# Performance work log

Hardware: AMD Instinct MI355X
Metric: run time of the kernel (lower is better)

Reference implementation:

```python
import jax, jax.numpy as jnp
import numpy as np

N = 65536      # total nodes in batched graph
E = 524288     # total edges (avg degree 8)
DIN = 128
DOUT = 128
G = 512        # number of graphs in the batch
NC = 10        # n_class


def _glorot(k, fi, fo):
    lim = np.sqrt(6.0 / (fi + fo)).astype(np.float32)
    return jax.random.uniform(k, (fi, fo), jnp.float32, -lim, lim)


def setup_inputs() -> dict:
    key = jax.random.key(0)
    ks = jax.random.split(key, 16)
    inp = {
        "hx": jax.random.normal(ks[0], (N, DIN), jnp.float32),
        "src": jax.random.randint(ks[1], (E,), 0, N),
        "dst": jax.random.randint(ks[2], (E,), 0, N),
        "graph_id": jnp.sort(jax.random.randint(ks[3], (N,), 0, G)),
        "num_graphs": G,
    }
    dims = [(DIN, DOUT)] + [(DOUT, DOUT)] * 5
    for i, (fi, fo) in enumerate(dims):
        inp[f"W{i+1}"] = _glorot(ks[4 + i], fi, fo)
        inp[f"b{i+1}"] = jnp.zeros((fo,), jnp.float32)
    inp["Wp1"] = _glorot(ks[10], DOUT, DOUT // 2)
    inp["bp1"] = jnp.zeros((DOUT // 2,), jnp.float32)
    inp["Wp2"] = _glorot(ks[11], DOUT // 2, NC)
    inp["bp2"] = jnp.zeros((NC,), jnp.float32)
    return inp


def reference(hx, src, dst, graph_id, num_graphs,
              W1, b1, W2, b2, W3, b3, W4, b4, W5, b5, W6, b6,
              Wp1, bp1, Wp2, bp2):
    n = hx.shape[0]
    ones_e = jnp.ones((src.shape[0],), jnp.float32)
    # DGL GraphConv norm='both': D_out^{-1/2} on src side, D_in^{-1/2} on dst side,
    # degrees clamped to min 1 (allow_zero_in_degree=True).
    deg_out = jax.ops.segment_sum(ones_e, src, num_segments=n)
    deg_in = jax.ops.segment_sum(ones_e, dst, num_segments=n)
    norm_src = jax.lax.rsqrt(jnp.maximum(deg_out, 1.0))[:, None]
    norm_dst = jax.lax.rsqrt(jnp.maximum(deg_in, 1.0))[:, None]

    def gconv(x, W, b):
        m = (x * norm_src)[src]                                  # [E, d] gather
        agg = jax.ops.segment_sum(m, dst, num_segments=n)        # scatter-add
        return (agg * norm_dst) @ W + b

    # 6 stacked conv layers, ReLU; dropout is identity in eval mode
    h = hx
    for W, b in ((W1, b1), (W2, b2), (W3, b3), (W4, b4), (W5, b5), (W6, b6)):
        h = jax.nn.relu(gconv(h, W, b))

    # dgl.mean_nodes: per-graph mean pooling
    pooled = jax.ops.segment_sum(h, graph_id, num_segments=num_graphs)
    cnt = jax.ops.segment_sum(jnp.ones((n,), jnp.float32), graph_id,
                              num_segments=num_graphs)
    pooled = pooled / jnp.maximum(cnt, 1.0)[:, None]

    # pred_lin MLP head
    scores = jax.nn.relu(pooled @ Wp1 + bp1) @ Wp2 + bp2
    # Note: the trailing update_all writes graph.ndata['h'] only (side effect),
    # it does not affect the returned scores, so it is omitted.
    return scores
```

## Files before the change

### kernel.cpp

```cpp
#include <hip/hip_runtime.h>
#include <hip/hip_bf16.h>

#define NN 65536
#define NE 524288
#define DF 128
#define NG 512
#define NCLS 10
#define NBLK 256
#define EPB (NE / NBLK)
#define EPT (EPB / 256)

typedef __bf16 bf16x8 __attribute__((ext_vector_type(8)));
typedef float f32x4 __attribute__((ext_vector_type(4)));
typedef ushort u16x8 __attribute__((ext_vector_type(8)));

__device__ __forceinline__ float bl(uint x) { return __uint_as_float(x << 16); }
__device__ __forceinline__ float bh(uint x) { return __uint_as_float(x & 0xffff0000u); }
__device__ __forceinline__ ushort f2b(float f) {
    uint u = __float_as_uint(f);
    return (ushort)((u + 0x7fffu + ((u >> 16) & 1u)) >> 16);
}


__global__ __launch_bounds__(256) void k_hist(
        const int* __restrict__ src, const int* __restrict__ dst,
        int* __restrict__ Md, int* __restrict__ Ms) {
    __shared__ int hd[256], hs[256];
    int t = threadIdx.x, b = blockIdx.x;
    hd[t] = 0; hs[t] = 0;
    __syncthreads();
    int base = b * EPB;
    for (int k = 0; k < EPT; k++) {
        int e = base + k * 256 + t;
        atomicAdd(&hd[dst[e] >> 8], 1);
        atomicAdd(&hs[src[e] >> 8], 1);
    }
    __syncthreads();
    Md[b * 256 + t] = hd[t];
    Ms[b * 256 + t] = hs[t];
}

__global__ __launch_bounds__(256) void k_colscan(
        const int* __restrict__ Md, const int* __restrict__ Ms,
        int* __restrict__ Bd, int* __restrict__ Bs,
        int* __restrict__ bbd, int* __restrict__ bbs) {
    __shared__ int tot[256];
    int t = threadIdx.x;
    const int* M = blockIdx.x ? Ms : Md;
    int* B = blockIdx.x ? Bs : Bd;
    int* bb = blockIdx.x ? bbs : bbd;
    int run = 0;
    #pragma unroll 16
    for (int b = 0; b < NBLK; b++) { B[b * 256 + t] = run; run += M[b * 256 + t]; }
    tot[t] = run;
    __syncthreads();
    if (t == 0) { int r = 0; for (int i = 0; i < 256; i++) { int c = tot[i]; tot[i] = r; r += c; } }
    __syncthreads();
    bb[t] = tot[t];
    if (t == 0) bb[256] = NE;
}

__global__ __launch_bounds__(256) void k_place(
        const int* __restrict__ src, const int* __restrict__ dst,
        const int* __restrict__ Bd, const int* __restrict__ bbd,
        const int* __restrict__ Bs, const int* __restrict__ bbs,
        uint* __restrict__ drec, ushort* __restrict__ srec) {
    __shared__ int cd[256], cs[256];
    int t = threadIdx.x, b = blockIdx.x;
    cd[t] = bbd[t] + Bd[b * 256 + t];
    cs[t] = bbs[t] + Bs[b * 256 + t];
    __syncthreads();
    int base = b * EPB;
    for (int k = 0; k < EPT; k++) {
        int e = base + k * 256 + t;
        int d = dst[e], s = src[e];
        int pd = atomicAdd(&cd[d >> 8], 1);
        drec[pd] = ((uint)s << 8) | (uint)(d & 255);
        int ps = atomicAdd(&cs[s >> 8], 1);
        srec[ps] = (ushort)(s & 255);
    }
}

__global__ __launch_bounds__(256) void k_bshist(
        const uint* __restrict__ drec, const int* __restrict__ bbd,
        const ushort* __restrict__ srec, const int* __restrict__ bbs,
        int* __restrict__ col, int* __restrict__ rp,
        float* __restrict__ nd, float* __restrict__ ns) {
    __shared__ int hist[256], cur[256], sc[256];
    __shared__ uint recs[4096];
    __shared__ int colst[4096];
    int t = threadIdx.x;
    if (blockIdx.x >= 256) {
        int b = blockIdx.x - 256;
        hist[t] = 0;
        __syncthreads();
        int s0 = bbs[b], e0 = bbs[b + 1];
        for (int i = s0 + t; i < e0; i += 256)
            atomicAdd(&hist[srec[i] & 255], 1);
        __syncthreads();
        ns[b * 256 + t] = rsqrtf((float)max(hist[t], 1));
        return;
    }
    int b = blockIdx.x;
    int s0 = bbd[b];
    int n = min(bbd[b + 1] - s0, 4096);
    hist[t] = 0;
    __syncthreads();
    for (int i = t; i < n; i += 256) {
        uint rc = drec[s0 + i];
        recs[i] = rc;
        atomicAdd(&hist[rc & 255u], 1);
    }
    __syncthreads();
    int v = hist[t];
    sc[t] = v;
    __syncthreads();
    for (int off = 1; off < 256; off <<= 1) {
        int x = (t >= off) ? sc[t - off] : 0;
        __syncthreads();
        sc[t] += x;
        __syncthreads();
    }
    int excl = sc[t] - v;
    rp[b * 256 + t] = s0 + excl;
    nd[b * 256 + t] = rsqrtf((float)max(v, 1));
    cur[t] = excl;
    __syncthreads();
    for (int i = t; i < n; i += 256) {
        uint rc = recs[i];
        int p = atomicAdd(&cur[rc & 255u], 1);
        colst[p] = (int)(rc >> 8);
    }
    __syncthreads();
    for (int i = t; i < n; i += 256) col[s0 + i] = colst[i];
    if (b == 0) {
        if (t == 0) rp[NN] = NE;
        if (t < 64) col[NE + t] = 0;
    }
}

__global__ __launch_bounds__(256) void k_scale_wconv(
        const float* __restrict__ hx, const float* __restrict__ ns,
        uint2* __restrict__ xs2,
        const float* __restrict__ W0, const float* __restrict__ W1,
        const float* __restrict__ W2, const float* __restrict__ W3,
        const float* __restrict__ W4, const float* __restrict__ W5,
        ushort* __restrict__ Wt) {
    if (blockIdx.x < 8192) {
        int i = blockIdx.x * 256 + threadIdx.x;
        float4 v = ((const float4*)hx)[i];
        float s = ns[i >> 5];
        uint2 o;
        o.x = (uint)f2b(v.x * s) | ((uint)f2b(v.y * s) << 16);
        o.y = (uint)f2b(v.z * s) | ((uint)f2b(v.w * s) << 16);
        xs2[i] = o;
    } else {
        int t = (blockIdx.x - 8192) * 256 + threadIdx.x;
        int l = t >> 14, r = t & 16383;
        const float* W = l == 0 ? W0 : l == 1 ? W1 : l == 2 ? W2
                       : l == 3 ? W3 : l == 4 ? W4 : W5;
        int n = r >> 7, k = r & 127;
        Wt[l * 16384 + n * 128 + k] = f2b(W[k * 128 + n]);
    }
}

#define ISSUE4(x0, x1, x2, x3, CR, K) { \
    int c0_ = __builtin_amdgcn_readlane((int)(CR), (K)); \
    int c1_ = __builtin_amdgcn_readlane((int)(CR), (K) + 1); \
    int c2_ = __builtin_amdgcn_readlane((int)(CR), (K) + 2); \
    int c3_ = __builtin_amdgcn_readlane((int)(CR), (K) + 3); \
    x0 = X32[(size_t)c0_ * 64 + lane]; \
    x1 = X32[(size_t)c1_ * 64 + lane]; \
    x2 = X32[(size_t)c2_ * 64 + lane]; \
    x3 = X32[(size_t)c3_ * 64 + lane]; }

#define FLUSHROWS(J) \
    while ((J) >= next_e && r < 15) { \
        *(float2*)&Af[r * 132 + 2 * lane] = make_float2(a0, a1); \
        a0 = 0.f; a1 = 0.f; r++; \
        next_e = __builtin_amdgcn_readlane(rpv, r + 1); }

#define PROC1(xv, J) { FLUSHROWS(J) \
    if ((J) < E) { a0 += bl(xv); a1 += bh(xv); } }

__global__ __launch_bounds__(64, 2) void k_fused(
        const uint* __restrict__ X32,
        const int* __restrict__ rp, const int* __restrict__ col,
        const float* __restrict__ nd, const float* __restrict__ ns,
        const uint4* __restrict__ Wg,
        const float* __restrict__ b, int do_scale,
        ushort* __restrict__ out) {
    __shared__ float Af[16 * 132];
    int lane = threadIdx.x;
    int rr = lane & 15;
    int q = lane >> 4;
    int nb = blockIdx.x * 16;

    int rpv = rp[nb + (lane < 16 ? lane : 16)];
    int S = __builtin_amdgcn_readlane(rpv, 0);
    int E = __builtin_amdgcn_readlane(rpv, 16);
    int r = 0;
    int next_e = __builtin_amdgcn_readlane(rpv, 1);
    float a0 = 0.f, a1 = 0.f;

    int c0 = col[S + rr];
    int cA = col[S + 16 + rr];

    uint xa0, xa1, xa2, xa3, xb0, xb1, xb2, xb3;
    uint xc0, xc1, xc2, xc3, xd0, xd1, xd2, xd3;
    int j = S;
    ISSUE4(xa0, xa1, xa2, xa3, c0, 0)
    ISSUE4(xb0, xb1, xb2, xb3, c0, 4)
    ISSUE4(xc0, xc1, xc2, xc3, c0, 8)
    ISSUE4(xd0, xd1, xd2, xd3, c0, 12)
    for (; j + 16 <= E; j += 16) {
        int cF = col[j + 32 + rr];
        PROC1(xa0, j)      PROC1(xa1, j + 1)  PROC1(xa2, j + 2)  PROC1(xa3, j + 3)
        ISSUE4(xa0, xa1, xa2, xa3, cA, 0)
        PROC1(xb0, j + 4)  PROC1(xb1, j + 5)  PROC1(xb2, j + 6)  PROC1(xb3, j + 7)
        ISSUE4(xb0, xb1, xb2, xb3, cA, 4)
        PROC1(xc0, j + 8)  PROC1(xc1, j + 9)  PROC1(xc2, j + 10) PROC1(xc3, j + 11)
        ISSUE4(xc0, xc1, xc2, xc3, cA, 8)
        PROC1(xd0, j + 12) PROC1(xd1, j + 13) PROC1(xd2, j + 14) PROC1(xd3, j + 15)
        ISSUE4(xd0, xd1, xd2, xd3, cA, 12)
        cA = cF;
    }
    PROC1(xa0, j)      PROC1(xa1, j + 1)  PROC1(xa2, j + 2)  PROC1(xa3, j + 3)
    PROC1(xb0, j + 4)  PROC1(xb1, j + 5)  PROC1(xb2, j + 6)  PROC1(xb3, j + 7)
    PROC1(xc0, j + 8)  PROC1(xc1, j + 9)  PROC1(xc2, j + 10) PROC1(xc3, j + 11)
    PROC1(xd0, j + 12) PROC1(xd1, j + 13) PROC1(xd2, j + 14) PROC1(xd3, j + 15)
    for (; r < 16; r++) {
        *(float2*)&Af[r * 132 + 2 * lane] = make_float2(a0, a1);
        a0 = 0.f; a1 = 0.f;
    }

    float ndv = nd[nb + rr];
    bf16x8 afr[4];
    #pragma unroll
    for (int ks = 0; ks < 4; ks++) {
        const f32x4* Afv = (const f32x4*)&Af[rr * 132 + ks * 32 + q * 8];
        f32x4 v0 = Afv[0], v1 = Afv[1];
        union { u16x8 u; bf16x8 f; } cv;
        cv.u[0] = f2b(v0[0] * ndv); cv.u[1] = f2b(v0[1] * ndv);
        cv.u[2] = f2b(v0[2] * ndv); cv.u[3] = f2b(v0[3] * ndv);
        cv.u[4] = f2b(v1[0] * ndv); cv.u[5] = f2b(v1[1] * ndv);
        cv.u[6] = f2b(v1[2] * ndv); cv.u[7] = f2b(v1[3] * ndv);
        afr[ks] = cv.f;
    }

    f32x4 cacc[8] = {};
    #pragma unroll
    for (int ks = 0; ks < 4; ks++) {
        #pragma unroll
        for (int ni = 0; ni < 8; ni++) {
            union { uint4 u; bf16x8 f; } bw;
            bw.u = Wg[(size_t)(ni * 16 + rr) * 16 + ks * 4 + q];
            cacc[ni] = __builtin_amdgcn_mfma_f32_16x16x32_bf16(
                afr[ks], bw.f, cacc[ni], 0, 0, 0);
        }
    }

    ushort* Cs = (ushort*)Af;
    float sc4[4];
    #pragma unroll
    for (int rg = 0; rg < 4; rg++)
        sc4[rg] = do_scale ? ns[nb + q * 4 + rg] : 1.f;
    #pragma unroll
    for (int ni = 0; ni < 8; ni++) {
        int c = ni * 16 + rr;
        float bb = b[c];
        #pragma unroll
        for (int rg = 0; rg < 4; rg++) {
            float v = fmaxf(cacc[ni][rg] + bb, 0.f) * sc4[rg];
            Cs[(q * 4 + rg) * 128 + c] = f2b(v);
        }
    }
    const uint4* Cs4 = (const uint4*)Cs;
    uint4* Og = (uint4*)(out + (size_t)nb * 128);
    #pragma unroll
    for (int it = 0; it < 4; it++)
        Og[it * 64 + lane] = Cs4[it * 64 + lane];
}

__global__ __launch_bounds__(256) void k_pool(
        const uint2* __restrict__ h2, const int* __restrict__ gid,
        float* __restrict__ pooled) {
    __shared__ int se[2];
    __shared__ float4 part[256];
    int g = blockIdx.x, t = threadIdx.x;
    if (t < 2) {
        int tgt = g + t;
        int lo = 0, hi = NN;
        while (lo < hi) { int mid = (lo + hi) >> 1; if (gid[mid] < tgt) lo = mid + 1; else hi = mid; }
        se[t] = lo;
    }
    __syncthreads();
    int s = se[0], e = se[1];
    int d2 = t & 31, qq = t >> 5;
    float4 acc = make_float4(0.f, 0.f, 0.f, 0.f);
    for (int i = s + qq; i < e; i += 8) {
        uint2 x = h2[(size_t)i * 32 + d2];
        acc.x += bl(x.x); acc.y += bh(x.x);
        acc.z += bl(x.y); acc.w += bh(x.y);
    }
    part[t] = acc;
    __syncthreads();
    if (t < 32) {
        float4 a = part[t];
        #pragma unroll
        for (int k = 1; k < 8; k++) {
            float4 p = part[t + 32 * k];
            a.x += p.x; a.y += p.y; a.z += p.z; a.w += p.w;
        }
        float inv = 1.f / fmaxf((float)(e - s), 1.f);
        ((float4*)(pooled + g * 128))[t] =
            make_float4(a.x * inv, a.y * inv, a.z * inv, a.w * inv);
    }
}

__global__ __launch_bounds__(64) void k_head(
        const float* __restrict__ pooled,
        const float* __restrict__ Wp1, const float* __restrict__ bp1,
        const float* __restrict__ Wp2, const float* __restrict__ bp2,
        float* __restrict__ scores) {
    __shared__ float p[128];
    __shared__ float t1[64];
    int g = blockIdx.x, t = threadIdx.x;
    p[t] = pooled[g * 128 + t];
    p[t + 64] = pooled[g * 128 + 64 + t];
    __syncthreads();
    float a = 0.f;
    for (int k = 0; k < 128; k++) a += p[k] * Wp1[k * 64 + t];
    t1[t] = fmaxf(a + bp1[t], 0.f);
    __syncthreads();
    if (t < NCLS) {
        float s = bp2[t];
        for (int k = 0; k < 64; k++) s += t1[k] * Wp2[k * NCLS + t];
        scores[g * NCLS + t] = s;
    }
}

extern "C" void kernel_launch(void* const* d_in, const int* in_sizes, int n_in,
                              void* d_out, int out_size, void* d_ws, size_t ws_size,
                              hipStream_t stream) {
    const float* hx  = (const float*)d_in[0];
    const int*   src = (const int*)d_in[1];
    const int*   dst = (const int*)d_in[2];
    const int*   gid = (const int*)d_in[3];
    const float* Ws[6], *bs[6];
    for (int l = 0; l < 6; l++) {
        Ws[l] = (const float*)d_in[5 + 2 * l];
        bs[l] = (const float*)d_in[6 + 2 * l];
    }
    const float* Wp1 = (const float*)d_in[17];
    const float* bp1 = (const float*)d_in[18];
    const float* Wp2 = (const float*)d_in[19];
    const float* bp2 = (const float*)d_in[20];
    float* scores = (float*)d_out;

    char* w = (char*)d_ws;
    ushort* xsA = (ushort*)w;     w += (size_t)NN * DF * 2;
    ushort* xsB = (ushort*)w;     w += (size_t)NN * DF * 2;
    ushort* Wt = (ushort*)w;      w += (size_t)6 * 128 * 128 * 2;
    int* Md   = (int*)w;          w += 256 * 256 * 4;
    int* Ms   = (int*)w;          w += 256 * 256 * 4;
    int* Bd   = (int*)w;          w += 256 * 256 * 4;
    int* Bs   = (int*)w;          w += 256 * 256 * 4;
    int* bbd  = (int*)w;          w += 257 * 4 + 12;
    int* bbs  = (int*)w;          w += 257 * 4 + 12;
    int* rp   = (int*)w;          w += (NN + 1) * 4 + 12;
    int* colv = (int*)w;          w += (NE + 64) * 4;
    float* ns   = (float*)w;      w += NN * 4;
    float* ndst = (float*)w;      w += NN * 4;
    float* pooled = (float*)w;    w += NG * DF * 4;
    uint*   drec = (uint*)xsB;
    ushort* srec = (ushort*)((char*)xsB + (size_t)NE * 4);

    k_hist<<<NBLK, 256, 0, stream>>>(src, dst, Md, Ms);
    k_colscan<<<2, 256, 0, stream>>>(Md, Ms, Bd, Bs, bbd, bbs);
    k_place<<<NBLK, 256, 0, stream>>>(src, dst, Bd, bbd, Bs, bbs, drec, srec);
    k_bshist<<<512, 256, 0, stream>>>(drec, bbd, srec, bbs, colv, rp, ndst, ns);
    k_scale_wconv<<<8192 + 384, 256, 0, stream>>>(
        hx, ns, (uint2*)xsA, Ws[0], Ws[1], Ws[2], Ws[3], Ws[4], Ws[5], Wt);

    ushort* cur = xsA;
    ushort* nxt = xsB;
    for (int l = 0; l < 6; l++) {
        k_fused<<<NN / 16, 64, 0, stream>>>(
            (const uint*)cur, rp, colv, ndst, ns,
            (const uint4*)(Wt + (size_t)l * 128 * 128), bs[l],
            (l < 5) ? 1 : 0, nxt);
        ushort* tmp = cur; cur = nxt; nxt = tmp;
    }

    k_pool<<<NG, 256, 0, stream>>>((const uint2*)cur, gid, pooled);
    k_head<<<NG, 64, 0, stream>>>(pooled, Wp1, bp1, Wp2, bp2, scores);
}
```

Measured before the change: 264.5 us.

## Stage edge placement through LDS for coalesced writes and fuse pool with head

The placement kernel now sorts each block's edges locally by destination bin, then by source bin, in shared memory. A prefix scan over the bin counts sets each edge's slot, so records are written to global memory in contiguous runs instead of as scattered per-edge atomic-slot stores. The pooling and MLP-head kernels are merged into one launch, which removes the intermediate pooled buffer and one kernel launch. The cost is extra LDS use, several barrier-heavy scans per block, and two passes over the edges.

```diff
diff --git a/kernel.cpp b/kernel.cpp
--- a/kernel.cpp
+++ b/kernel.cpp
@@ -65,19 +65,77 @@
         const int* __restrict__ Bd, const int* __restrict__ bbd,
         const int* __restrict__ Bs, const int* __restrict__ bbs,
         uint* __restrict__ drec, ushort* __restrict__ srec) {
-    __shared__ int cd[256], cs[256];
+    __shared__ int cnt[256], scn[256];
+    __shared__ uint stage[EPB];
+    __shared__ uchar sbin[EPB];
     int t = threadIdx.x, b = blockIdx.x;
-    cd[t] = bbd[t] + Bd[b * 256 + t];
-    cs[t] = bbs[t] + Bs[b * 256 + t];
-    __syncthreads();
     int base = b * EPB;
+    int dv[EPT], sv[EPT], rk[EPT];
+    #pragma unroll
     for (int k = 0; k < EPT; k++) {
         int e = base + k * 256 + t;
-        int d = dst[e], s = src[e];
-        int pd = atomicAdd(&cd[d >> 8], 1);
-        drec[pd] = ((uint)s << 8) | (uint)(d & 255);
-        int ps = atomicAdd(&cs[s >> 8], 1);
-        srec[ps] = (ushort)(s & 255);
+        dv[k] = dst[e]; sv[k] = src[e];
+    }
+
+    cnt[t] = 0;
+    __syncthreads();
+    #pragma unroll
+    for (int k = 0; k < EPT; k++) rk[k] = atomicAdd(&cnt[dv[k] >> 8], 1);
+    __syncthreads();
+    int v = cnt[t];
+    scn[t] = v;
+    __syncthreads();
+    for (int off = 1; off < 256; off <<= 1) {
+        int x = (t >= off) ? scn[t - off] : 0;
+        __syncthreads();
+        scn[t] += x;
+        __syncthreads();
+    }
+    #pragma unroll
+    for (int k = 0; k < EPT; k++) {
+        int bin = dv[k] >> 8;
+        int slot = (scn[bin] - cnt[bin]) + rk[k];
+        stage[slot] = ((uint)sv[k] << 8) | (uint)(dv[k] & 255);
+        sbin[slot] = (uchar)bin;
+    }
+    __syncthreads();
+    #pragma unroll
+    for (int k = 0; k < EPT; k++) {
+        int i = k * 256 + t;
+        int bin = sbin[i];
+        int local = i - (scn[bin] - cnt[bin]);
+        drec[bbd[bin] + Bd[b * 256 + bin] + local] = stage[i];
+    }
+    __syncthreads();
+
+    cnt[t] = 0;
+    __syncthreads();
+    #pragma unroll
+    for (int k = 0; k < EPT; k++) rk[k] = atomicAdd(&cnt[sv[k] >> 8], 1);
+    __syncthreads();
+    v = cnt[t];
+    scn[t] = v;
+    __syncthreads();
+    for (int off = 1; off < 256; off <<= 1) {
+        int x = (t >= off) ? scn[t - off] : 0;
+        __syncthreads();
+        scn[t] += x;
+        __syncthreads();
+    }
+    #pragma unroll
+    for (int k = 0; k < EPT; k++) {
+        int bin = sv[k] >> 8;
+        int slot = (scn[bin] - cnt[bin]) + rk[k];
+        stage[slot] = (uint)(sv[k] & 255);
+        sbin[slot] = (uchar)bin;
+    }
+    __syncthreads();
+    #pragma unroll
+    for (int k = 0; k < EPT; k++) {
+        int i = k * 256 + t;
+        int bin = sbin[i];
+        int local = i - (scn[bin] - cnt[bin]);
+        srec[bbs[bin] + Bs[b * 256 + bin] + local] = (ushort)stage[i];
     }
 }
 
@@ -282,11 +340,15 @@
         Og[it * 64 + lane] = Cs4[it * 64 + lane];
 }
 
-__global__ __launch_bounds__(256) void k_pool(
+__global__ __launch_bounds__(256) void k_poolhead(
         const uint2* __restrict__ h2, const int* __restrict__ gid,
-        float* __restrict__ pooled) {
+        const float* __restrict__ Wp1, const float* __restrict__ bp1,
+        const float* __restrict__ Wp2, const float* __restrict__ bp2,
+        float* __restrict__ scores) {
     __shared__ int se[2];
     __shared__ float4 part[256];
+    __shared__ float p[128];
+    __shared__ float t1[64];
     int g = blockIdx.x, t = threadIdx.x;
     if (t < 2) {
         int tgt = g + t;
@@ -309,34 +371,24 @@
         float4 a = part[t];
         #pragma unroll
         for (int k = 1; k < 8; k++) {
-            float4 p = part[t + 32 * k];
-            a.x += p.x; a.y += p.y; a.z += p.z; a.w += p.w;
+            float4 pp = part[t + 32 * k];
+            a.x += pp.x; a.y += pp.y; a.z += pp.z; a.w += pp.w;
         }
         float inv = 1.f / fmaxf((float)(e - s), 1.f);
-        ((float4*)(pooled + g * 128))[t] =
-            make_float4(a.x * inv, a.y * inv, a.z * inv, a.w * inv);
-    }
-}
-
-__global__ __launch_bounds__(64) void k_head(
-        const float* __restrict__ pooled,
-        const float* __restrict__ Wp1, const float* __restrict__ bp1,
-        const float* __restrict__ Wp2, const float* __restrict__ bp2,
-        float* __restrict__ scores) {
-    __shared__ float p[128];
-    __shared__ float t1[64];
-    int g = blockIdx.x, t = threadIdx.x;
-    p[t] = pooled[g * 128 + t];
-    p[t + 64] = pooled[g * 128 + 64 + t];
-    __syncthreads();
-    float a = 0.f;
-    for (int k = 0; k < 128; k++) a += p[k] * Wp1[k * 64 + t];
-    t1[t] = fmaxf(a + bp1[t], 0.f);
+        p[4 * t + 0] = a.x * inv; p[4 * t + 1] = a.y * inv;
+        p[4 * t + 2] = a.z * inv; p[4 * t + 3] = a.w * inv;
+    }
+    __syncthreads();
+    if (t < 64) {
+        float a = 0.f;
+        for (int k = 0; k < 128; k++) a += p[k] * Wp1[k * 64 + t];
+        t1[t] = fmaxf(a + bp1[t], 0.f);
+    }
     __syncthreads();
     if (t < NCLS) {
-        float s = bp2[t];
-        for (int k = 0; k < 64; k++) s += t1[k] * Wp2[k * NCLS + t];
-        scores[g * NCLS + t] = s;
+        float sacc = bp2[t];
+        for (int k = 0; k < 64; k++) sacc += t1[k] * Wp2[k * NCLS + t];
+        scores[g * NCLS + t] = sacc;
     }
 }
 
@@ -372,7 +424,6 @@
     int* colv = (int*)w;          w += (NE + 64) * 4;
     float* ns   = (float*)w;      w += NN * 4;
     float* ndst = (float*)w;      w += NN * 4;
-    float* pooled = (float*)w;    w += NG * DF * 4;
     uint*   drec = (uint*)xsB;
     ushort* srec = (ushort*)((char*)xsB + (size_t)NE * 4);
 
@@ -393,6 +444,6 @@
         ushort* tmp = cur; cur = nxt; nxt = tmp;
     }
 
-    k_pool<<<NG, 256, 0, stream>>>((const uint2*)cur, gid, pooled);
-    k_head<<<NG, 64, 0, stream>>>(pooled, Wp1, bp1, Wp2, bp2, scores);
-}
+    k_poolhead<<<NG, 256, 0, stream>>>((const uint2*)cur, gid,
+                                       Wp1, bp1, Wp2, bp2, scores);
+}
```

After: 261.5 us. About the same (-1.1%).
